# Kernel tuning notes

Hardware: AMD Instinct MI355X
Metric: run time of the kernel (lower is better)

Reference implementation:

```python
import jax, jax.numpy as jnp
import numpy as np


def setup_inputs() -> dict:
    key = jax.random.key(0)
    k1, k2 = jax.random.split(key)
    B, C, H, W, T = 8, 256, 64, 64, 512
    F_s = jax.random.normal(k1, (B, C, H, W), dtype=jnp.float32)
    F_t = jax.random.normal(k2, (B, T, C), dtype=jnp.float32)
    return {"F_s": F_s, "F_t": F_t}


def reference(F_s, F_t):
    B, C, H, W = F_s.shape
    T = F_t.shape[1]
    # [B, HW, C] spatial tokens
    F_s_t = jnp.transpose(F_s, (0, 2, 3, 1)).reshape(B, H * W, C)
    # scores [B, HW, T], scaled by sqrt(T) (softmax over last axis)
    A = jnp.einsum('bnc,btc->bnt', F_s_t, F_t) / jnp.sqrt(jnp.float32(T))
    A = jax.nn.softmax(A, axis=-1)
    # A^T @ F_s_t -> updated text tokens [B, T, C]
    F_t_updated = jnp.einsum('bnt,bnc->btc', A, F_s_t)
    # A @ F_t -> spatial update [B, HW, C]
    F_s_t_update = jnp.einsum('bnt,btc->bnc', A, F_t)
    F_s_t_update = jnp.transpose(F_s_t_update.reshape(B, H, W, C), (0, 3, 1, 2))
    F_s_updated = F_s + F_s_t_update
    return (F_s_updated, F_t_updated)
```

## Files before the change

kernel.cpp:

```cpp
#include <hip/hip_runtime.h>
#include <hip/hip_bf16.h>
#include <stdint.h>


typedef __attribute__((ext_vector_type(8))) short short8v;
typedef __attribute__((ext_vector_type(4))) float float4v;

#define MFMA16(a, b, c) __builtin_amdgcn_mfma_f32_16x16x32_bf16(a, b, c, 0, 0, 0)
#define SCALE 0.04419417382415922f

static __device__ __forceinline__ unsigned short f2bf(float f) {
  union { float f; uint32_t u; } v; v.f = f;
  uint32_t r = v.u + 0x7fffu + ((v.u >> 16) & 1u);
  return (unsigned short)(r >> 16);
}
static __device__ __forceinline__ float bf2f(unsigned short u) {
  union { uint32_t u; float f; } v; v.u = (uint32_t)u << 16;
  return v.f;
}

static __device__ __forceinline__ void gload16(const void* g, void* l) {
  __builtin_amdgcn_global_load_lds(
      (const __attribute__((address_space(1))) void*)g,
      (__attribute__((address_space(3))) void*)l, 16, 0, 0);
}

__global__ __launch_bounds__(256) void k_cast_transpose(
    const float* __restrict__ src, unsigned short* __restrict__ dstC,
    unsigned short* __restrict__ dstT, int R, int Cd) {
  __shared__ unsigned short tile[32][33];
  const size_t zoff = (size_t)blockIdx.z * R * Cd;
  const float* s = src + zoff;
  unsigned short* dc = dstC + zoff;
  unsigned short* dt = dstT + zoff;
  const int c0 = blockIdx.x * 32, r0 = blockIdx.y * 32;
  const int tid = threadIdx.x;
  const int r = tid >> 3, c4 = (tid & 7) * 4;

  float4 v = *(const float4*)&s[(size_t)(r0 + r) * Cd + c0 + c4];
  ushort4 bq;
  bq.x = f2bf(v.x); bq.y = f2bf(v.y); bq.z = f2bf(v.z); bq.w = f2bf(v.w);
  *(ushort4*)&dc[(size_t)(r0 + r) * Cd + c0 + c4] = bq;
  tile[r][c4 + 0] = bq.x; tile[r][c4 + 1] = bq.y;
  tile[r][c4 + 2] = bq.z; tile[r][c4 + 3] = bq.w;
  __syncthreads();
  ushort4 o;
  o.x = tile[c4 + 0][r]; o.y = tile[c4 + 1][r];
  o.z = tile[c4 + 2][r]; o.w = tile[c4 + 3][r];
  *(ushort4*)&dt[(size_t)(c0 + r) * R + r0 + c4] = o;
}

__global__ __launch_bounds__(512) void k_attn(
    const unsigned short* __restrict__ Qg, const unsigned short* __restrict__ Kg,
    const unsigned short* __restrict__ VTg, const unsigned short* __restrict__ QTg,
    float* __restrict__ out0, unsigned short* __restrict__ PTg) {
  __shared__ char smem[163840];

  const int tid = threadIdx.x;
  const int wave = tid >> 6, lane = tid & 63;
  const int l16 = lane & 15, lhi = lane >> 4;
  const int b = blockIdx.x & 7, nb = blockIdx.x >> 3;
  const int n0w = nb * 128 + wave * 16;
  const int cx = (l16 & 7) << 4;
  const int cx2 = (l16 & 3) << 4;

  const unsigned short* Qb = Qg + (size_t)b * 4096 * 256;
  const char* Kb = (const char*)(Kg + (size_t)b * 512 * 256);
  const char* VTb = (const char*)(VTg + (size_t)b * 256 * 512);
  char* Psb = smem + 32768 + wave * 16384;

  short8v aQ[8];
#pragma unroll
  for (int kc = 0; kc < 8; kc++)
    aQ[kc] = *(const short8v*)(Qb + (size_t)(n0w + l16) * 256 + kc * 32 + lhi * 8);

  float4v acc[32];
#pragma unroll
  for (int tt = 0; tt < 32; tt++) acc[tt] = (float4v)0.f;

#define STAGE_K(c_, buf_) do {                                              \
    const char* src_ = Kb + (c_) * 16384;                                   \
    _Pragma("unroll")                                                       \
    for (int i = 0; i < 2; i++) {                                           \
      const int off = (tid + i * 512) * 16;                                 \
      gload16(src_ + (off ^ (((off >> 9) & 7) << 4)),                       \
              smem + (buf_) * 16384 + off);                                 \
    } } while (0)

#define STAGE_V(c_, buf_) do {                                              \
    _Pragma("unroll")                                                       \
    for (int i = 0; i < 2; i++) {                                           \
      const int off = (tid + i * 512) * 16;                                 \
      const int r_ = off >> 6, ic_ = off & 63;                              \
      gload16(VTb + (size_t)r_ * 1024 + (c_) * 64 + (ic_ ^ ((r_ & 3) << 4)), \
              smem + (buf_) * 16384 + off);                                 \
    } } while (0)

  STAGE_K(0, 0);
  __syncthreads();
#pragma unroll
  for (int c = 0; c < 16; c++) {
    const int buf = c & 1;
    if (c < 15) STAGE_K(c + 1, buf ^ 1);
#pragma unroll
    for (int ti = 0; ti < 2; ti++) {
      const int row = ti * 16 + l16;
      const char* rb = smem + buf * 16384 + row * 512;
#pragma unroll
      for (int kc = 0; kc < 8; kc++) {
        short8v bf = *(const short8v*)(rb + ((kc * 64 + lhi * 16) ^ cx));
        acc[c * 2 + ti] = MFMA16(aQ[kc], bf, acc[c * 2 + ti]);
      }
    }
    __syncthreads();
  }

  STAGE_V(0, 0);

  float mx[4], sm[4];
#pragma unroll
  for (int r = 0; r < 4; r++) {
    float m = acc[0][r];
#pragma unroll
    for (int tt = 1; tt < 32; tt++) m = fmaxf(m, acc[tt][r]);
    m = fmaxf(m, __shfl_xor(m, 1));
    m = fmaxf(m, __shfl_xor(m, 2));
    m = fmaxf(m, __shfl_xor(m, 4));
    m = fmaxf(m, __shfl_xor(m, 8));
    mx[r] = m;
  }
#pragma unroll
  for (int r = 0; r < 4; r++) {
    float s = 0.f;
#pragma unroll
    for (int tt = 0; tt < 32; tt++) {
      float p = __expf((acc[tt][r] - mx[r]) * SCALE);
      acc[tt][r] = p;
      s += p;
    }
    s += __shfl_xor(s, 1); s += __shfl_xor(s, 2);
    s += __shfl_xor(s, 4); s += __shfl_xor(s, 8);
    sm[r] = 1.0f / s;
  }

#pragma unroll
  for (int tt = 0; tt < 32; tt++)
#pragma unroll
    for (int r = 0; r < 4; r++) {
      const int q = lhi * 4 + r, t = tt * 16 + l16;
      *(unsigned short*)(Psb + ((q * 1024 + t * 2) ^ ((q & 7) << 4))) =
          f2bf(acc[tt][r] * sm[r]);
    }

  {
    unsigned short* PTb = PTg + (size_t)b * 512 * 4096;
#pragma unroll
    for (int it = 0; it < 8; it++) {
      const int t = it * 64 + lane;
      unsigned short tmp[16];
#pragma unroll
      for (int q = 0; q < 16; q++)
        tmp[q] = *(const unsigned short*)(Psb + ((q * 1024 + t * 2) ^ ((q & 7) << 4)));
      *(int4*)(PTb + (size_t)t * 4096 + n0w) = *(int4*)&tmp[0];
      *(int4*)(PTb + (size_t)t * 4096 + n0w + 8) = *(int4*)&tmp[8];
    }
  }
  __syncthreads();

  float4v oacc[16];
#pragma unroll
  for (int ct = 0; ct < 16; ct++) oacc[ct] = (float4v)0.f;

#pragma unroll
  for (int c = 0; c < 16; c++) {
    const int buf = c & 1;
    short8v pb = *(const short8v*)(Psb + ((l16 * 1024 + c * 64 + lhi * 16) ^ cx));
    if (c < 15) STAGE_V(c + 1, buf ^ 1);
#pragma unroll
    for (int ct = 0; ct < 16; ct++) {
      const int row = ct * 16 + l16;
      const char* rb = smem + buf * 16384 + row * 64;
      short8v av = *(const short8v*)(rb + ((lhi * 16) ^ cx2));
      oacc[ct] = MFMA16(av, pb, oacc[ct]);
    }
    __syncthreads();
  }

  const unsigned short* QTb = QTg + (size_t)b * 256 * 4096;
  float* o0 = out0 + (size_t)b * 256 * 4096;
#pragma unroll
  for (int ct = 0; ct < 16; ct++)
#pragma unroll
    for (int r = 0; r < 4; r++) {
      const int cgl = ct * 16 + lhi * 4 + r;
      const size_t off = (size_t)cgl * 4096 + n0w + l16;
      o0[off] = oacc[ct][r] + bf2f(QTb[off]);
    }
#undef STAGE_K
#undef STAGE_V
}

__global__ __launch_bounds__(256, 2) void k_ptq(
    const unsigned short* __restrict__ PTg, const unsigned short* __restrict__ QTg,
    float* __restrict__ part) {
  __shared__ char smem[65536];

  const int tid = threadIdx.x;
  const int wave = tid >> 6, lane = tid & 63;
  const int l16 = lane & 15, lhi = lane >> 4;
  const int bid = blockIdx.x;
  const int t0 = (bid >> 6) * 64;
  const int grp = bid & 63;
  const int b = grp & 7, ksl = grp >> 3;
  const int cx = (l16 & 7) << 4;

  const unsigned short* PTrow =
      PTg + ((size_t)(b * 512 + t0 + wave * 16 + l16)) * 4096 + ksl * 512 + lhi * 8;
  const char* QTb = (const char*)(QTg + (size_t)b * 256 * 4096 + ksl * 512);

#define STAGE_Q(c_, buf_) do {                                              \
    _Pragma("unroll")                                                       \
    for (int i = 0; i < 8; i++) {                                           \
      const int off = (tid + i * 256) * 16;                                 \
      const int r_ = off >> 7, ic_ = off & 127;                             \
      gload16(QTb + (size_t)r_ * 8192 + (c_) * 128 + (ic_ ^ ((r_ & 7) << 4)), \
              smem + (buf_) * 32768 + off);                                 \
    } } while (0)

  float4v acc[16];
#pragma unroll
  for (int ct = 0; ct < 16; ct++) acc[ct] = (float4v)0.f;

  STAGE_Q(0, 0);
  __syncthreads();
#pragma unroll
  for (int c = 0; c < 8; c++) {
    const int buf = c & 1;
    short8v pa0 = *(const short8v*)(PTrow + c * 64);
    short8v pa1 = *(const short8v*)(PTrow + c * 64 + 32);
    if (c < 7) STAGE_Q(c + 1, buf ^ 1);
#pragma unroll
    for (int ct = 0; ct < 16; ct++) {
      const int row = ct * 16 + l16;
      const char* rb = smem + buf * 32768 + row * 128;
      short8v b0 = *(const short8v*)(rb + ((lhi * 16) ^ cx));
      acc[ct] = MFMA16(pa0, b0, acc[ct]);
      short8v b1 = *(const short8v*)(rb + ((64 + lhi * 16) ^ cx));
      acc[ct] = MFMA16(pa1, b1, acc[ct]);
    }
    __syncthreads();
  }

  float* pout = part + (((size_t)ksl * 8 + b) * 512 + t0 + wave * 16) * 256;
#pragma unroll
  for (int ct = 0; ct < 16; ct++)
#pragma unroll
    for (int r = 0; r < 4; r++)
      pout[(lhi * 4 + r) * 256 + ct * 16 + l16] = acc[ct][r];
#undef STAGE_Q
}

__global__ __launch_bounds__(256) void k_red(
    const float* __restrict__ part, float* __restrict__ out1) {
  const int g = blockIdx.x * 256 + threadIdx.x;
  float4 s = *(const float4*)(part + (size_t)g * 4);
#pragma unroll
  for (int ksl = 1; ksl < 8; ksl++) {
    float4 v = *(const float4*)(part + (size_t)ksl * 1048576 + (size_t)g * 4);
    s.x += v.x; s.y += v.y; s.z += v.z; s.w += v.w;
  }
  *(float4*)(out1 + (size_t)g * 4) = s;
}

extern "C" void kernel_launch(void* const* d_in, const int* in_sizes, int n_in,
                              void* d_out, int out_size, void* d_ws, size_t ws_size,
                              hipStream_t stream) {
  const float* Fs = (const float*)d_in[0];
  const float* Ft = (const float*)d_in[1];
  float* out0 = (float*)d_out;
  float* out1 = out0 + (size_t)8 * 256 * 4096;

  unsigned short* ws = (unsigned short*)d_ws;
  unsigned short* Q  = ws;
  unsigned short* QT = Q + 8388608;
  unsigned short* K  = QT + 8388608;
  unsigned short* VT = K + 1048576;
  unsigned short* PT = VT + 1048576;
  float* part = (float*)(PT + 16777216);

  k_cast_transpose<<<dim3(128, 8, 8), 256, 0, stream>>>(Fs, QT, Q, 256, 4096);
  k_cast_transpose<<<dim3(8, 16, 8), 256, 0, stream>>>(Ft, K, VT, 512, 256);
  k_attn<<<dim3(256), 512, 0, stream>>>(Q, K, VT, QT, out0, PT);
  k_ptq<<<dim3(512), 256, 0, stream>>>(PT, QT, part);
  k_red<<<dim3(1024), 256, 0, stream>>>(part, out1);
}
```

Baseline: 87.48 us.

## Shrink attention blocks to four waves and stream probabilities through small LDS tiles

The attention kernel drops from 512-thread blocks with 160KB of LDS to 256-thread blocks with 80KB, which allows two blocks per CU, and launches twice as many blocks. The normalized probabilities are packed into registers as bf16 pairs. They are then written to LDS per 64-token chunk, interleaved with the P·V MFMA loop and the PT global stores, instead of staging the full 16x512 tile per wave. K and V stage in larger 32KB chunks, with the first V chunk prefetched during the last K step. The aim is better latency hiding through occupancy and overlap. The costs are more register pressure from the 64 packed words and more barriers per block.

```diff
diff --git a/kernel.cpp b/kernel.cpp
--- a/kernel.cpp
+++ b/kernel.cpp
@@ -50,24 +50,40 @@
   *(ushort4*)&dt[(size_t)(c0 + r) * R + r0 + c4] = o;
 }
 
-__global__ __launch_bounds__(512) void k_attn(
+__global__ __launch_bounds__(256, 2) void k_attn(
     const unsigned short* __restrict__ Qg, const unsigned short* __restrict__ Kg,
     const unsigned short* __restrict__ VTg, const unsigned short* __restrict__ QTg,
     float* __restrict__ out0, unsigned short* __restrict__ PTg) {
-  __shared__ char smem[163840];
+  __shared__ char smem[81920];
 
   const int tid = threadIdx.x;
   const int wave = tid >> 6, lane = tid & 63;
   const int l16 = lane & 15, lhi = lane >> 4;
   const int b = blockIdx.x & 7, nb = blockIdx.x >> 3;
-  const int n0w = nb * 128 + wave * 16;
+  const int n0w = nb * 64 + wave * 16;
   const int cx = (l16 & 7) << 4;
-  const int cx2 = (l16 & 3) << 4;
 
   const unsigned short* Qb = Qg + (size_t)b * 4096 * 256;
   const char* Kb = (const char*)(Kg + (size_t)b * 512 * 256);
   const char* VTb = (const char*)(VTg + (size_t)b * 256 * 512);
-  char* Psb = smem + 32768 + wave * 16384;
+
+#define STAGE_K8(e_, buf_) do {                                             \
+    const char* src_ = Kb + (e_) * 32768;                                   \
+    _Pragma("unroll")                                                       \
+    for (int i = 0; i < 8; i++) {                                           \
+      const int off = (tid + i * 256) * 16;                                 \
+      gload16(src_ + (off ^ (((off >> 9) & 7) << 4)),                       \
+              smem + (buf_) * 32768 + off);                                 \
+    } } while (0)
+
+#define STAGE_VT(t_, buf_) do {                                             \
+    _Pragma("unroll")                                                       \
+    for (int i = 0; i < 8; i++) {                                           \
+      const int off = (tid + i * 256) * 16;                                 \
+      const int r_ = off >> 7, ic_ = off & 127;                             \
+      gload16(VTb + (size_t)r_ * 1024 + (t_) * 128 + (ic_ ^ ((r_ & 7) << 4)), \
+              smem + (buf_) * 32768 + off);                                 \
+    } } while (0)
 
   short8v aQ[8];
 #pragma unroll
@@ -78,44 +94,25 @@
 #pragma unroll
   for (int tt = 0; tt < 32; tt++) acc[tt] = (float4v)0.f;
 
-#define STAGE_K(c_, buf_) do {                                              \
-    const char* src_ = Kb + (c_) * 16384;                                   \
-    _Pragma("unroll")                                                       \
-    for (int i = 0; i < 2; i++) {                                           \
-      const int off = (tid + i * 512) * 16;                                 \
-      gload16(src_ + (off ^ (((off >> 9) & 7) << 4)),                       \
-              smem + (buf_) * 16384 + off);                                 \
-    } } while (0)
-
-#define STAGE_V(c_, buf_) do {                                              \
-    _Pragma("unroll")                                                       \
-    for (int i = 0; i < 2; i++) {                                           \
-      const int off = (tid + i * 512) * 16;                                 \
-      const int r_ = off >> 6, ic_ = off & 63;                              \
-      gload16(VTb + (size_t)r_ * 1024 + (c_) * 64 + (ic_ ^ ((r_ & 3) << 4)), \
-              smem + (buf_) * 16384 + off);                                 \
-    } } while (0)
-
-  STAGE_K(0, 0);
+  STAGE_K8(0, 0);
   __syncthreads();
 #pragma unroll
-  for (int c = 0; c < 16; c++) {
-    const int buf = c & 1;
-    if (c < 15) STAGE_K(c + 1, buf ^ 1);
-#pragma unroll
-    for (int ti = 0; ti < 2; ti++) {
+  for (int e = 0; e < 8; e++) {
+    const int buf = e & 1;
+    if (e < 7) STAGE_K8(e + 1, buf ^ 1);
+    else       STAGE_VT(0, 0);
+#pragma unroll
+    for (int ti = 0; ti < 4; ti++) {
       const int row = ti * 16 + l16;
-      const char* rb = smem + buf * 16384 + row * 512;
+      const char* rb = smem + buf * 32768 + row * 512;
 #pragma unroll
       for (int kc = 0; kc < 8; kc++) {
         short8v bf = *(const short8v*)(rb + ((kc * 64 + lhi * 16) ^ cx));
-        acc[c * 2 + ti] = MFMA16(aQ[kc], bf, acc[c * 2 + ti]);
+        acc[e * 4 + ti] = MFMA16(aQ[kc], bf, acc[e * 4 + ti]);
       }
     }
-    __syncthreads();
-  }
-
-  STAGE_V(0, 0);
+    if (e < 7) __syncthreads();
+  }
 
   float mx[4], sm[4];
 #pragma unroll
@@ -143,47 +140,58 @@
     sm[r] = 1.0f / s;
   }
 
+  uint32_t pk[64];
 #pragma unroll
   for (int tt = 0; tt < 32; tt++)
 #pragma unroll
-    for (int r = 0; r < 4; r++) {
-      const int q = lhi * 4 + r, t = tt * 16 + l16;
-      *(unsigned short*)(Psb + ((q * 1024 + t * 2) ^ ((q & 7) << 4))) =
-          f2bf(acc[tt][r] * sm[r]);
-    }
-
-  {
-    unsigned short* PTb = PTg + (size_t)b * 512 * 4096;
-#pragma unroll
-    for (int it = 0; it < 8; it++) {
-      const int t = it * 64 + lane;
-      unsigned short tmp[16];
-#pragma unroll
-      for (int q = 0; q < 16; q++)
-        tmp[q] = *(const unsigned short*)(Psb + ((q * 1024 + t * 2) ^ ((q & 7) << 4)));
-      *(int4*)(PTb + (size_t)t * 4096 + n0w) = *(int4*)&tmp[0];
-      *(int4*)(PTb + (size_t)t * 4096 + n0w + 8) = *(int4*)&tmp[8];
-    }
-  }
-  __syncthreads();
+    for (int h = 0; h < 2; h++)
+      pk[tt * 2 + h] = (uint32_t)f2bf(acc[tt][2 * h] * sm[2 * h]) |
+                       ((uint32_t)f2bf(acc[tt][2 * h + 1] * sm[2 * h + 1]) << 16);
 
   float4v oacc[16];
 #pragma unroll
   for (int ct = 0; ct < 16; ct++) oacc[ct] = (float4v)0.f;
 
-#pragma unroll
-  for (int c = 0; c < 16; c++) {
-    const int buf = c & 1;
-    short8v pb = *(const short8v*)(Psb + ((l16 * 1024 + c * 64 + lhi * 16) ^ cx));
-    if (c < 15) STAGE_V(c + 1, buf ^ 1);
+  unsigned short* PTb = PTg + (size_t)b * 512 * 4096;
+
+#pragma unroll
+  for (int tau = 0; tau < 8; tau++) {
+    const int buf = tau & 1;
+    __syncthreads();
+    if (tau < 7) STAGE_VT(tau + 1, buf ^ 1);
+
+    char* Psb = smem + 65536 + buf * 8192 + wave * 2048;
+#pragma unroll
+    for (int s = 0; s < 4; s++)
+#pragma unroll
+      for (int r = 0; r < 4; r++) {
+        const int q = lhi * 4 + r, t2 = s * 16 + l16;
+        const uint32_t w = pk[(tau * 4 + s) * 2 + (r >> 1)];
+        *(unsigned short*)(Psb + ((q * 128 + t2 * 2) ^ ((q & 7) << 4))) =
+            (unsigned short)(w >> ((r & 1) * 16));
+      }
+
+    short8v pb0 = *(const short8v*)(Psb + ((l16 * 128 + lhi * 16) ^ cx));
+    short8v pb1 = *(const short8v*)(Psb + ((l16 * 128 + 64 + lhi * 16) ^ cx));
 #pragma unroll
     for (int ct = 0; ct < 16; ct++) {
       const int row = ct * 16 + l16;
-      const char* rb = smem + buf * 16384 + row * 64;
-      short8v av = *(const short8v*)(rb + ((lhi * 16) ^ cx2));
-      oacc[ct] = MFMA16(av, pb, oacc[ct]);
-    }
-    __syncthreads();
+      const char* rb = smem + buf * 32768 + row * 128;
+      short8v a0 = *(const short8v*)(rb + ((lhi * 16) ^ cx));
+      oacc[ct] = MFMA16(a0, pb0, oacc[ct]);
+      short8v a1 = *(const short8v*)(rb + ((64 + lhi * 16) ^ cx));
+      oacc[ct] = MFMA16(a1, pb1, oacc[ct]);
+    }
+
+    {
+      const int t2 = lane;
+      unsigned short tmp[16];
+#pragma unroll
+      for (int q = 0; q < 16; q++)
+        tmp[q] = *(const unsigned short*)(Psb + ((q * 128 + t2 * 2) ^ ((q & 7) << 4)));
+      *(int4*)(PTb + (size_t)(tau * 64 + t2) * 4096 + n0w) = *(int4*)&tmp[0];
+      *(int4*)(PTb + (size_t)(tau * 64 + t2) * 4096 + n0w + 8) = *(int4*)&tmp[8];
+    }
   }
 
   const unsigned short* QTb = QTg + (size_t)b * 256 * 4096;
@@ -196,8 +204,8 @@
       const size_t off = (size_t)cgl * 4096 + n0w + l16;
       o0[off] = oacc[ct][r] + bf2f(QTb[off]);
     }
-#undef STAGE_K
-#undef STAGE_V
+#undef STAGE_K8
+#undef STAGE_VT
 }
 
 __global__ __launch_bounds__(256, 2) void k_ptq(
@@ -290,7 +298,7 @@
 
   k_cast_transpose<<<dim3(128, 8, 8), 256, 0, stream>>>(Fs, QT, Q, 256, 4096);
   k_cast_transpose<<<dim3(8, 16, 8), 256, 0, stream>>>(Ft, K, VT, 512, 256);
-  k_attn<<<dim3(256), 512, 0, stream>>>(Q, K, VT, QT, out0, PT);
+  k_attn<<<dim3(512), 256, 0, stream>>>(Q, K, VT, QT, out0, PT);
   k_ptq<<<dim3(512), 256, 0, stream>>>(PT, QT, part);
   k_red<<<dim3(1024), 256, 0, stream>>>(part, out1);
 }
```

Result: faster. 83.08 us (-5.0%).

## Stream attention flash-style without max, defer normalization, store partials in bf16

Applied to the files above, without the earlier changes.

The attention kernel now processes K/V chunks in a single streaming loop with a three-slot LDS ring buffer. Each chunk's scores are exponentiated without max subtraction and immediately multiplied into V, and the output is normalized afterward by a row-sum inverse that is also written to global memory. Unnormalized P^T is stored, and k_ptq rescales it by the inverse sums before its MFMA. Block size and LDS shrink so more blocks fit per CU, and the split-K partials are written in bf16 to halve reduction traffic. Dropping the max subtraction risks exp overflow for large scores, and the bf16 partials lose precision.

```diff
diff --git a/kernel.cpp b/kernel.cpp
--- a/kernel.cpp
+++ b/kernel.cpp
@@ -50,141 +50,128 @@
   *(ushort4*)&dt[(size_t)(c0 + r) * R + r0 + c4] = o;
 }
 
-__global__ __launch_bounds__(512) void k_attn(
+__global__ __launch_bounds__(256, 3) void k_attn(
     const unsigned short* __restrict__ Qg, const unsigned short* __restrict__ Kg,
     const unsigned short* __restrict__ VTg, const unsigned short* __restrict__ QTg,
-    float* __restrict__ out0, unsigned short* __restrict__ PTg) {
-  __shared__ char smem[163840];
+    float* __restrict__ out0, unsigned short* __restrict__ PTg,
+    float* __restrict__ invlg) {
+  __shared__ char smem[53248];
 
   const int tid = threadIdx.x;
   const int wave = tid >> 6, lane = tid & 63;
   const int l16 = lane & 15, lhi = lane >> 4;
   const int b = blockIdx.x & 7, nb = blockIdx.x >> 3;
-  const int n0w = nb * 128 + wave * 16;
+  const int n0w = nb * 64 + wave * 16;
   const int cx = (l16 & 7) << 4;
   const int cx2 = (l16 & 3) << 4;
 
   const unsigned short* Qb = Qg + (size_t)b * 4096 * 256;
   const char* Kb = (const char*)(Kg + (size_t)b * 512 * 256);
   const char* VTb = (const char*)(VTg + (size_t)b * 256 * 512);
-  char* Psb = smem + 32768 + wave * 16384;
+  char* Ps = smem + 49152 + wave * 1024;
+
+#define STAGE_K(i_) do {                                                    \
+    const char* src_ = Kb + (i_) * 16384;                                   \
+    char* dst_ = smem + ((2 * (i_)) % 3) * 16384;                           \
+    _Pragma("unroll")                                                       \
+    for (int u = 0; u < 4; u++) {                                           \
+      const int off = (tid + u * 256) * 16;                                 \
+      gload16(src_ + (off ^ (((off >> 9) & 7) << 4)), dst_ + off);          \
+    } } while (0)
+
+#define STAGE_V(i_) do {                                                    \
+    char* dst_ = smem + ((2 * (i_) + 1) % 3) * 16384;                       \
+    _Pragma("unroll")                                                       \
+    for (int u = 0; u < 4; u++) {                                           \
+      const int off = (tid + u * 256) * 16;                                 \
+      const int r_ = off >> 6, ic_ = off & 63;                              \
+      gload16(VTb + (size_t)r_ * 1024 + (i_) * 64 + (ic_ ^ ((r_ & 3) << 4)), \
+              dst_ + off);                                                  \
+    } } while (0)
 
   short8v aQ[8];
 #pragma unroll
   for (int kc = 0; kc < 8; kc++)
     aQ[kc] = *(const short8v*)(Qb + (size_t)(n0w + l16) * 256 + kc * 32 + lhi * 8);
 
-  float4v acc[32];
-#pragma unroll
-  for (int tt = 0; tt < 32; tt++) acc[tt] = (float4v)0.f;
-
-#define STAGE_K(c_, buf_) do {                                              \
-    const char* src_ = Kb + (c_) * 16384;                                   \
-    _Pragma("unroll")                                                       \
-    for (int i = 0; i < 2; i++) {                                           \
-      const int off = (tid + i * 512) * 16;                                 \
-      gload16(src_ + (off ^ (((off >> 9) & 7) << 4)),                       \
-              smem + (buf_) * 16384 + off);                                 \
-    } } while (0)
-
-#define STAGE_V(c_, buf_) do {                                              \
-    _Pragma("unroll")                                                       \
-    for (int i = 0; i < 2; i++) {                                           \
-      const int off = (tid + i * 512) * 16;                                 \
-      const int r_ = off >> 6, ic_ = off & 63;                              \
-      gload16(VTb + (size_t)r_ * 1024 + (c_) * 64 + (ic_ ^ ((r_ & 3) << 4)), \
-              smem + (buf_) * 16384 + off);                                 \
-    } } while (0)
-
-  STAGE_K(0, 0);
-  __syncthreads();
-#pragma unroll
-  for (int c = 0; c < 16; c++) {
-    const int buf = c & 1;
-    if (c < 15) STAGE_K(c + 1, buf ^ 1);
-#pragma unroll
-    for (int ti = 0; ti < 2; ti++) {
-      const int row = ti * 16 + l16;
-      const char* rb = smem + buf * 16384 + row * 512;
+  float4v oacc[16];
+#pragma unroll
+  for (int ct = 0; ct < 16; ct++) oacc[ct] = (float4v)0.f;
+  float lrun[4] = {0.f, 0.f, 0.f, 0.f};
+
+  unsigned short* PTb = PTg + (size_t)b * 512 * 4096;
+
+  STAGE_K(0); STAGE_V(0);
+#pragma unroll
+  for (int i = 0; i < 16; i++) {
+    asm volatile("s_waitcnt vmcnt(4)" ::: "memory");
+    __builtin_amdgcn_s_barrier();
+    if (i < 15) STAGE_K(i + 1);
+    float4v s0 = (float4v)0.f, s1 = (float4v)0.f;
+    {
+      const char* kb = smem + ((2 * i) % 3) * 16384;
+      const char* rb0 = kb + l16 * 512;
+      const char* rb1 = kb + (16 + l16) * 512;
 #pragma unroll
       for (int kc = 0; kc < 8; kc++) {
-        short8v bf = *(const short8v*)(rb + ((kc * 64 + lhi * 16) ^ cx));
-        acc[c * 2 + ti] = MFMA16(aQ[kc], bf, acc[c * 2 + ti]);
+        short8v bf0 = *(const short8v*)(rb0 + ((kc * 64 + lhi * 16) ^ cx));
+        s0 = MFMA16(aQ[kc], bf0, s0);
+        short8v bf1 = *(const short8v*)(rb1 + ((kc * 64 + lhi * 16) ^ cx));
+        s1 = MFMA16(aQ[kc], bf1, s1);
       }
     }
-    __syncthreads();
+    asm volatile("s_waitcnt lgkmcnt(0)" ::: "memory");
+
+    if (i < 15) asm volatile("s_waitcnt vmcnt(4)" ::: "memory");
+    else        asm volatile("s_waitcnt vmcnt(0)" ::: "memory");
+    __builtin_amdgcn_s_barrier();
+    if (i < 15) STAGE_V(i + 1);
+#pragma unroll
+    for (int r = 0; r < 4; r++) {
+      const int q = lhi * 4 + r;
+      float p0 = __expf(s0[r] * SCALE);
+      float p1 = __expf(s1[r] * SCALE);
+      lrun[r] += p0 + p1;
+      *(unsigned short*)(Ps + ((q * 64 + l16 * 2) ^ ((q & 3) << 4))) = f2bf(p0);
+      *(unsigned short*)(Ps + ((q * 64 + (16 + l16) * 2) ^ ((q & 3) << 4))) = f2bf(p1);
+    }
+    asm volatile("s_waitcnt lgkmcnt(0)" ::: "memory");
+    {
+      short8v pb = *(const short8v*)(Ps + ((l16 * 64 + lhi * 16) ^ cx2));
+      const char* vb = smem + ((2 * i + 1) % 3) * 16384;
+#pragma unroll
+      for (int ct = 0; ct < 16; ct++) {
+        const char* rb = vb + (ct * 16 + l16) * 64;
+        short8v av = *(const short8v*)(rb + ((lhi * 16) ^ cx2));
+        oacc[ct] = MFMA16(av, pb, oacc[ct]);
+      }
+    }
+    {
+      const int t2 = lane & 31, half = lane >> 5;
+      unsigned short tmp[8];
+#pragma unroll
+      for (int j = 0; j < 8; j++) {
+        const int q = half * 8 + j;
+        tmp[j] = *(const unsigned short*)(Ps + ((q * 64 + t2 * 2) ^ ((q & 3) << 4)));
+      }
+      *(int4*)(PTb + (size_t)(32 * i + t2) * 4096 + n0w + half * 8) = *(int4*)tmp;
+    }
+    asm volatile("s_waitcnt lgkmcnt(0)" ::: "memory");
   }
 
-  STAGE_V(0, 0);
-
-  float mx[4], sm[4];
 #pragma unroll
   for (int r = 0; r < 4; r++) {
-    float m = acc[0][r];
-#pragma unroll
-    for (int tt = 1; tt < 32; tt++) m = fmaxf(m, acc[tt][r]);
-    m = fmaxf(m, __shfl_xor(m, 1));
-    m = fmaxf(m, __shfl_xor(m, 2));
-    m = fmaxf(m, __shfl_xor(m, 4));
-    m = fmaxf(m, __shfl_xor(m, 8));
-    mx[r] = m;
+    float l = lrun[r];
+    l += __shfl_xor(l, 1); l += __shfl_xor(l, 2);
+    l += __shfl_xor(l, 4); l += __shfl_xor(l, 8);
+    lrun[r] = 1.0f / l;
   }
-#pragma unroll
-  for (int r = 0; r < 4; r++) {
-    float s = 0.f;
-#pragma unroll
-    for (int tt = 0; tt < 32; tt++) {
-      float p = __expf((acc[tt][r] - mx[r]) * SCALE);
-      acc[tt][r] = p;
-      s += p;
-    }
-    s += __shfl_xor(s, 1); s += __shfl_xor(s, 2);
-    s += __shfl_xor(s, 4); s += __shfl_xor(s, 8);
-    sm[r] = 1.0f / s;
-  }
-
-#pragma unroll
-  for (int tt = 0; tt < 32; tt++)
-#pragma unroll
-    for (int r = 0; r < 4; r++) {
-      const int q = lhi * 4 + r, t = tt * 16 + l16;
-      *(unsigned short*)(Psb + ((q * 1024 + t * 2) ^ ((q & 7) << 4))) =
-          f2bf(acc[tt][r] * sm[r]);
-    }
-
-  {
-    unsigned short* PTb = PTg + (size_t)b * 512 * 4096;
-#pragma unroll
-    for (int it = 0; it < 8; it++) {
-      const int t = it * 64 + lane;
-      unsigned short tmp[16];
-#pragma unroll
-      for (int q = 0; q < 16; q++)
-        tmp[q] = *(const unsigned short*)(Psb + ((q * 1024 + t * 2) ^ ((q & 7) << 4)));
-      *(int4*)(PTb + (size_t)t * 4096 + n0w) = *(int4*)&tmp[0];
-      *(int4*)(PTb + (size_t)t * 4096 + n0w + 8) = *(int4*)&tmp[8];
-    }
-  }
-  __syncthreads();
-
-  float4v oacc[16];
-#pragma unroll
-  for (int ct = 0; ct < 16; ct++) oacc[ct] = (float4v)0.f;
-
-#pragma unroll
-  for (int c = 0; c < 16; c++) {
-    const int buf = c & 1;
-    short8v pb = *(const short8v*)(Psb + ((l16 * 1024 + c * 64 + lhi * 16) ^ cx));
-    if (c < 15) STAGE_V(c + 1, buf ^ 1);
-#pragma unroll
-    for (int ct = 0; ct < 16; ct++) {
-      const int row = ct * 16 + l16;
-      const char* rb = smem + buf * 16384 + row * 64;
-      short8v av = *(const short8v*)(rb + ((lhi * 16) ^ cx2));
-      oacc[ct] = MFMA16(av, pb, oacc[ct]);
-    }
-    __syncthreads();
-  }
+  const int srcl = (l16 >> 2) << 4;
+  float va = __shfl(lrun[0], srcl), vb2 = __shfl(lrun[1], srcl);
+  float vc = __shfl(lrun[2], srcl), vd = __shfl(lrun[3], srcl);
+  const int rs = l16 & 3;
+  float myinv = rs == 0 ? va : (rs == 1 ? vb2 : (rs == 2 ? vc : vd));
+  if (lane < 16) invlg[(size_t)b * 4096 + n0w + lane] = myinv;
 
   const unsigned short* QTb = QTg + (size_t)b * 256 * 4096;
   float* o0 = out0 + (size_t)b * 256 * 4096;
@@ -194,7 +181,7 @@
     for (int r = 0; r < 4; r++) {
       const int cgl = ct * 16 + lhi * 4 + r;
       const size_t off = (size_t)cgl * 4096 + n0w + l16;
-      o0[off] = oacc[ct][r] + bf2f(QTb[off]);
+      o0[off] = oacc[ct][r] * myinv + bf2f(QTb[off]);
     }
 #undef STAGE_K
 #undef STAGE_V
@@ -202,7 +189,7 @@
 
 __global__ __launch_bounds__(256, 2) void k_ptq(
     const unsigned short* __restrict__ PTg, const unsigned short* __restrict__ QTg,
-    float* __restrict__ part) {
+    const float* __restrict__ invlg, unsigned short* __restrict__ part) {
   __shared__ char smem[65536];
 
   const int tid = threadIdx.x;
@@ -217,11 +204,12 @@
   const unsigned short* PTrow =
       PTg + ((size_t)(b * 512 + t0 + wave * 16 + l16)) * 4096 + ksl * 512 + lhi * 8;
   const char* QTb = (const char*)(QTg + (size_t)b * 256 * 4096 + ksl * 512);
+  const float* ivb = invlg + (size_t)b * 4096 + ksl * 512 + lhi * 8;
 
 #define STAGE_Q(c_, buf_) do {                                              \
     _Pragma("unroll")                                                       \
-    for (int i = 0; i < 8; i++) {                                           \
-      const int off = (tid + i * 256) * 16;                                 \
+    for (int u = 0; u < 8; u++) {                                           \
+      const int off = (tid + u * 256) * 16;                                 \
       const int r_ = off >> 7, ic_ = off & 127;                             \
       gload16(QTb + (size_t)r_ * 8192 + (c_) * 128 + (ic_ ^ ((r_ & 7) << 4)), \
               smem + (buf_) * 32768 + off);                                 \
@@ -238,6 +226,19 @@
     const int buf = c & 1;
     short8v pa0 = *(const short8v*)(PTrow + c * 64);
     short8v pa1 = *(const short8v*)(PTrow + c * 64 + 32);
+    {
+      float4 iv0 = *(const float4*)(ivb + c * 64);
+      float4 iv1 = *(const float4*)(ivb + c * 64 + 4);
+      float4 iv2 = *(const float4*)(ivb + c * 64 + 32);
+      float4 iv3 = *(const float4*)(ivb + c * 64 + 36);
+      const float f0[8] = {iv0.x, iv0.y, iv0.z, iv0.w, iv1.x, iv1.y, iv1.z, iv1.w};
+      const float f1[8] = {iv2.x, iv2.y, iv2.z, iv2.w, iv3.x, iv3.y, iv3.z, iv3.w};
+#pragma unroll
+      for (int j = 0; j < 8; j++) {
+        pa0[j] = (short)f2bf(bf2f((unsigned short)pa0[j]) * f0[j]);
+        pa1[j] = (short)f2bf(bf2f((unsigned short)pa1[j]) * f1[j]);
+      }
+    }
     if (c < 7) STAGE_Q(c + 1, buf ^ 1);
 #pragma unroll
     for (int ct = 0; ct < 16; ct++) {
@@ -251,25 +252,31 @@
     __syncthreads();
   }
 
-  float* pout = part + (((size_t)ksl * 8 + b) * 512 + t0 + wave * 16) * 256;
+  unsigned short* pout = part + (((size_t)ksl * 8 + b) * 512 + t0 + wave * 16) * 256;
 #pragma unroll
   for (int ct = 0; ct < 16; ct++)
 #pragma unroll
     for (int r = 0; r < 4; r++)
-      pout[(lhi * 4 + r) * 256 + ct * 16 + l16] = acc[ct][r];
+      pout[(lhi * 4 + r) * 256 + ct * 16 + l16] = f2bf(acc[ct][r]);
 #undef STAGE_Q
 }
 
 __global__ __launch_bounds__(256) void k_red(
-    const float* __restrict__ part, float* __restrict__ out1) {
-  const int g = blockIdx.x * 256 + threadIdx.x;
-  float4 s = *(const float4*)(part + (size_t)g * 4);
-#pragma unroll
-  for (int ksl = 1; ksl < 8; ksl++) {
-    float4 v = *(const float4*)(part + (size_t)ksl * 1048576 + (size_t)g * 4);
-    s.x += v.x; s.y += v.y; s.z += v.z; s.w += v.w;
+    const unsigned short* __restrict__ part, float* __restrict__ out1) {
+  const size_t g = (size_t)(blockIdx.x * 256 + threadIdx.x) * 8;
+  float s[8];
+#pragma unroll
+  for (int j = 0; j < 8; j++) s[j] = 0.f;
+#pragma unroll
+  for (int ksl = 0; ksl < 8; ksl++) {
+    short8v v = *(const short8v*)(part + (size_t)ksl * 1048576 + g);
+#pragma unroll
+    for (int j = 0; j < 8; j++) s[j] += bf2f((unsigned short)v[j]);
   }
-  *(float4*)(out1 + (size_t)g * 4) = s;
+  float4 o0 = {s[0], s[1], s[2], s[3]};
+  float4 o1 = {s[4], s[5], s[6], s[7]};
+  *(float4*)(out1 + g) = o0;
+  *(float4*)(out1 + g + 4) = o1;
 }
 
 extern "C" void kernel_launch(void* const* d_in, const int* in_sizes, int n_in,
@@ -286,11 +293,12 @@
   unsigned short* K  = QT + 8388608;
   unsigned short* VT = K + 1048576;
   unsigned short* PT = VT + 1048576;
-  float* part = (float*)(PT + 16777216);
+  unsigned short* part = PT + 16777216;
+  float* invl = (float*)(part + 8388608);
 
   k_cast_transpose<<<dim3(128, 8, 8), 256, 0, stream>>>(Fs, QT, Q, 256, 4096);
   k_cast_transpose<<<dim3(8, 16, 8), 256, 0, stream>>>(Ft, K, VT, 512, 256);
-  k_attn<<<dim3(256), 512, 0, stream>>>(Q, K, VT, QT, out0, PT);
-  k_ptq<<<dim3(512), 256, 0, stream>>>(PT, QT, part);
-  k_red<<<dim3(1024), 256, 0, stream>>>(part, out1);
-}
+  k_attn<<<dim3(512), 256, 0, stream>>>(Q, K, VT, QT, out0, PT, invl);
+  k_ptq<<<dim3(512), 256, 0, stream>>>(PT, QT, invl, part);
+  k_red<<<dim3(512), 256, 0, stream>>>(part, out1);
+}
```

New measurement: 119.5 us. 36.6% more time.
